# Kernel tuning notes

Measured on AMD Instinct MI355X. Metric: run time of the kernel, lower is better.

## Reference

```python
import jax, jax.numpy as jnp
import numpy as np

N = 60000      # total nodes
D = 300        # feature dim
R = 5          # num relations == num bases
E = 1_000_000  # edges
S = 25000      # last_idx_senses
G = 50000      # last_idx_globals
BATCH = 32


def setup_inputs() -> dict:
    key = jax.random.key(0)
    ks = jax.random.split(key, 12)
    x = jax.random.normal(ks[0], (N, D), dtype=jnp.float32)
    edge_index = jax.random.randint(ks[1], (2, E), 0, N, dtype=jnp.int32)
    edge_type = jax.random.randint(ks[2], (E,), 0, R, dtype=jnp.int32)
    current_node_index = jax.random.randint(ks[3], (BATCH,), 0, N, dtype=jnp.int32)
    scale = 1.0 / np.sqrt(D)
    # RGCNConv basis decomposition params (num_bases == num_relations)
    basis = jax.random.normal(ks[4], (R, D, D), dtype=jnp.float32) * scale
    comp = jax.random.normal(ks[5], (R, R), dtype=jnp.float32) * scale
    root = jax.random.normal(ks[6], (D, D), dtype=jnp.float32) * scale
    bias = jnp.zeros((D,), dtype=jnp.float32)
    # heads
    w_global = jax.random.normal(ks[7], (G - S, D), dtype=jnp.float32) * scale
    b_global = jnp.zeros((G - S,), dtype=jnp.float32)
    w_sense = jax.random.normal(ks[8], (S, D), dtype=jnp.float32) * scale
    b_sense = jnp.zeros((S,), dtype=jnp.float32)
    return {
        "x": x, "edge_index": edge_index, "edge_type": edge_type,
        "current_node_index": current_node_index,
        "basis": basis, "comp": comp, "root": root, "bias": bias,
        "w_global": w_global, "b_global": b_global,
        "w_sense": w_sense, "b_sense": b_sense,
    }


def reference(x, edge_index, edge_type, current_node_index,
              basis, comp, root, bias,
              w_global, b_global, w_sense, b_sense):
    src, dst = edge_index[0], edge_index[1]
    # Combined segment id over (dst node, relation): mean-aggregate source
    # features per (node, relation), then apply the per-relation transform
    # (mean(x_j) @ W_r == mean(x_j @ W_r); matches PyG RGCNConv aggr='mean').
    seg = dst * R + edge_type                      # [E]
    msg_sum = jax.ops.segment_sum(x[src], seg, num_segments=N * R)  # [N*R, D]
    cnt = jax.ops.segment_sum(jnp.ones((E,), jnp.float32), seg, num_segments=N * R)
    mean = msg_sum.reshape(N, R, D) / jnp.maximum(cnt.reshape(N, R, 1), 1.0)
    # basis decomposition: W_r = sum_b comp[r,b] * basis[b]
    W = jnp.einsum('rb,bij->rij', comp, basis)     # [R, D, D]
    agg = jnp.einsum('nrd,rde->ne', mean, W)       # [N, D]
    h = jax.nn.relu(agg + x @ root + bias)         # [N, D]
    hc = h[current_node_index]                     # [B, D]
    logits_global = hc @ w_global.T + b_global     # [B, G-S]
    logits_sense = hc @ w_sense.T + b_sense        # [B, S]
    return (jax.nn.log_softmax(logits_global, axis=-1),
            jax.nn.log_softmax(logits_sense, axis=-1))
```

## Files before the change

### kernel.cpp

```cpp
#include <hip/hip_runtime.h>
#include <hip/hip_bf16.h>
#include <math.h>

#define NN 60000
#define D 300
#define R 5
#define NE 1000000
#define B 32
#define NG 25000
#define NS 25000
#define NROWS 50000
#define HCP 304
#define NBLK 1563

typedef __bf16 bf16x8 __attribute__((ext_vector_type(8)));
typedef float f32x16 __attribute__((ext_vector_type(16)));


__global__ void zero_ws(float4* __restrict__ p) {
    int i = blockIdx.x * 256 + threadIdx.x;
    if (i < 14441) p[i] = float4{0.f, 0.f, 0.f, 0.f};
}

__global__ __launch_bounds__(256) void scan_accum(
        const int* __restrict__ ei, const int* __restrict__ et,
        const int* __restrict__ cur, const float* __restrict__ x,
        float* __restrict__ wsum, float* __restrict__ wcnt) {
    __shared__ unsigned int tbl[32];
    __shared__ int curl[B];
    __shared__ int lcnt;
    __shared__ int2 loc[64];
    int tid = threadIdx.x;
    if (tid < 32) tbl[tid] = 0u;
    if (tid == 0) lcnt = 0;
    __syncthreads();
    if (tid < B) {
        int c = cur[tid];
        curl[tid] = c;
        atomicOr(&tbl[(c >> 5) & 31], 1u << (c & 31));
    }
    __syncthreads();
    long base = ((long)blockIdx.x * 256 + tid) * 4;
    if (base < NE) {
        int ds[4];
        if (base + 4 <= NE) {
            int4 d4 = *(const int4*)(ei + NE + base);
            ds[0] = d4.x; ds[1] = d4.y; ds[2] = d4.z; ds[3] = d4.w;
        } else {
            for (int k = 0; k < 4; ++k) ds[k] = (base + k < NE) ? ei[NE + base + k] : -1;
        }
        #pragma unroll
        for (int k = 0; k < 4; ++k) {
            int dst = ds[k];
            if (dst < 0) continue;
            if (!(tbl[(dst >> 5) & 31] & (1u << (dst & 31)))) continue;
            int e = (int)base + k;
            int r = -1, s = 0;
            for (int b = 0; b < B; ++b) {
                if (dst == curl[b]) {
                    if (r < 0) { r = et[e]; s = ei[e]; }
                    int slot = b * R + r;
                    atomicAdd(&wcnt[slot], 1.0f);
                    int p = atomicAdd(&lcnt, 1);
                    if (p < 64) loc[p] = int2{s, slot};
                }
            }
        }
    }
    __syncthreads();
    int n = lcnt; if (n > 64) n = 64;
    for (int m = 0; m < n; ++m) {
        int2 pr = loc[m];
        const float* xs = x + (long)pr.x * D;
        float* sm = wsum + (long)pr.y * D;
        for (int t = tid; t < D; t += 256) atomicAdd(&sm[t], xs[t]);
    }
}

__global__ __launch_bounds__(320) void rgcn_hc(
        const float* __restrict__ x, const int* __restrict__ cur,
        const float* __restrict__ comp, const float* __restrict__ root,
        const float* __restrict__ basis, const float* __restrict__ bias,
        const float* __restrict__ wsum, const float* __restrict__ wcnt,
        float* __restrict__ hcf, int* __restrict__ done, __bf16* __restrict__ hcb) {
    int kc = blockIdx.x, t = threadIdx.x;
    __shared__ float uL[B * 50];
    __shared__ float cmp[R * R];
    __shared__ float inv[B * R];
    __shared__ int curlS[B];
    __shared__ int lastFlag;
    if (t < R * R) cmp[t] = comp[t];
    if (t < B * R) inv[t] = 1.0f / fmaxf(wcnt[t], 1.0f);
    if (t < B) curlS[t] = cur[t];
    __syncthreads();
    int d0 = kc * 50;
    if (kc < 6) {
        for (int i = t; i < B * 50; i += 320) {
            int b = i / 50, dd = i - b * 50;
            uL[i] = x[(long)curlS[b] * D + d0 + dd];
        }
    } else {
        int g0 = d0 - 300;
        int bb = g0 / 300, t0 = g0 - bb * 300;
        for (int i = t; i < B * 50; i += 320) {
            int b = i / 50, dd = i - b * 50;
            float a = 0.f;
            #pragma unroll
            for (int r = 0; r < R; ++r)
                a = fmaf(cmp[r * R + bb] * inv[b * R + r], wsum[((long)b * R + r) * D + t0 + dd], a);
            uL[i] = a;
        }
    }
    __syncthreads();
    const float* Mb = (kc < 6) ? (root + (long)d0 * D) : (basis + (long)(d0 - 300) * D);
    if (t < D) {
        float acc[B] = {};
        #pragma unroll 5
        for (int i = 0; i < 50; ++i) {
            float m = Mb[(long)i * D + t];
            #pragma unroll
            for (int b = 0; b < B; ++b) acc[b] = fmaf(uL[b * 50 + i], m, acc[b]);
        }
        for (int b = 0; b < B; ++b) atomicAdd(&hcf[b * D + t], acc[b]);
    }
    __syncthreads();
    if (t == 0) {
        __threadfence();
        int p = atomicAdd(done, 1);
        lastFlag = (p == 35);
    }
    __syncthreads();
    if (!lastFlag) return;
    __threadfence();
    for (int i = t; i < B * HCP; i += 320) {
        int b = i / HCP, tt = i - b * HCP;
        float a = 0.f;
        if (tt < D) {
            a = atomicAdd(&hcf[b * D + tt], 0.0f) + bias[tt];
            a = fmaxf(a, 0.f);
        }
        hcb[i] = (__bf16)a;
    }
}

__device__ inline void online_upd(float& m, float& s, float v) {
    if (v > m) { s = s * __expf(m - v) + 1.0f; m = v; }
    else       { s += __expf(v - m); }
}
__device__ inline void online_merge(float& m, float& s, float om, float os) {
    float M = fmaxf(m, om);
    s = s * __expf(m - M) + os * __expf(om - M);
    m = M;
}

__global__ __launch_bounds__(64) void head_gemm_mfma(
    const __bf16* __restrict__ hcb, const float* __restrict__ wg, const float* __restrict__ bg,
    const float* __restrict__ wsn, const float* __restrict__ bsn,
    float* __restrict__ out, float2* __restrict__ pm2) {
    int l = threadIdx.x;
    int j0 = blockIdx.x * 32;
    int lm = l & 31, lh = l >> 5;

    bf16x8 bfrag[19];
    const __bf16* hrow = hcb + lm * HCP + lh * 8;
    #pragma unroll
    for (int s = 0; s < 19; ++s) bfrag[s] = *(const bf16x8*)(hrow + 16 * s);

    int row = j0 + lm; if (row >= NROWS) row = NROWS - 1;
    const float* wrow = ((row < NG) ? (wg + (long)row * D) : (wsn + (long)(row - NG) * D)) + lh * 8;

    f32x16 acc = {};
    #pragma unroll
    for (int s = 0; s < 18; ++s) {
        float4 w0 = *(const float4*)(wrow + 16 * s);
        float4 w1 = *(const float4*)(wrow + 16 * s + 4);
        bf16x8 a;
        a[0] = (__bf16)w0.x; a[1] = (__bf16)w0.y; a[2] = (__bf16)w0.z; a[3] = (__bf16)w0.w;
        a[4] = (__bf16)w1.x; a[5] = (__bf16)w1.y; a[6] = (__bf16)w1.z; a[7] = (__bf16)w1.w;
        acc = __builtin_amdgcn_mfma_f32_32x32x16_bf16(a, bfrag[s], acc, 0, 0, 0);
    }
    {
        float4 w0, w1;
        if (lh == 0) {
            w0 = *(const float4*)(wrow + 288);
            w1 = *(const float4*)(wrow + 292);
        } else {
            w0 = *(const float4*)(wrow + 288);
            w1 = float4{0.f, 0.f, 0.f, 0.f};
        }
        bf16x8 a;
        a[0] = (__bf16)w0.x; a[1] = (__bf16)w0.y; a[2] = (__bf16)w0.z; a[3] = (__bf16)w0.w;
        a[4] = (__bf16)w1.x; a[5] = (__bf16)w1.y; a[6] = (__bf16)w1.z; a[7] = (__bf16)w1.w;
        acc = __builtin_amdgcn_mfma_f32_32x32x16_bf16(a, bfrag[18], acc, 0, 0, 0);
    }

    int b = lm;
    float m0 = -3.0e38f, s0 = 0.f, m1 = -3.0e38f, s1 = 0.f;
    #pragma unroll
    for (int r = 0; r < 16; ++r) {
        int j = j0 + (r & 3) + 8 * (r >> 2) + 4 * lh;
        if (j >= NROWS) continue;
        float bv = (j < NG) ? bg[j] : bsn[j - NG];
        float v = acc[r] + bv;
        float* op = (j < NG) ? (out + (long)b * NG + j)
                             : (out + (long)B * NG + (long)b * NS + (j - NG));
        *op = v;
        if (j < NG) online_upd(m0, s0, v); else online_upd(m1, s1, v);
    }
    float om0 = __shfl_xor(m0, 32), os0 = __shfl_xor(s0, 32);
    float om1 = __shfl_xor(m1, 32), os1 = __shfl_xor(s1, 32);
    online_merge(m0, s0, om0, os0);
    online_merge(m1, s1, om1, os1);
    if (lh == 0) {
        pm2[(long)b * NBLK + blockIdx.x]       = float2{m0, s0};
        pm2[(long)(B + b) * NBLK + blockIdx.x] = float2{m1, s1};
    }
}

__global__ __launch_bounds__(256) void sub_lse(float* __restrict__ out,
                                               const float2* __restrict__ pm2) {
    int row = blockIdx.x / 25, c = blockIdx.x % 25;
    int tid = threadIdx.x;
    const float2* pr = pm2 + (long)row * NBLK;
    float m = -3.0e38f, s = 0.f;
    for (int i = tid; i < NBLK; i += 256) {
        float2 e = pr[i];
        online_merge(m, s, e.x, e.y);
    }
    #pragma unroll
    for (int o = 32; o; o >>= 1) {
        float om = __shfl_xor(m, o), os = __shfl_xor(s, o);
        online_merge(m, s, om, os);
    }
    __shared__ float sm[4], ss[4];
    __shared__ float lseS;
    if ((tid & 63) == 0) { sm[tid >> 6] = m; ss[tid >> 6] = s; }
    __syncthreads();
    if (tid == 0) {
        float M = sm[0], S = ss[0];
        for (int w = 1; w < 4; ++w) online_merge(M, S, sm[w], ss[w]);
        lseS = M + __logf(S);
    }
    __syncthreads();
    float lse = lseS;
    float4* o4 = (float4*)out + (long)row * 6250 + c * 250;
    if (tid < 250) {
        float4 v = o4[tid];
        v.x -= lse; v.y -= lse; v.z -= lse; v.w -= lse;
        o4[tid] = v;
    }
}

extern "C" void kernel_launch(void* const* d_in, const int* in_sizes, int n_in,
                              void* d_out, int out_size, void* d_ws, size_t ws_size,
                              hipStream_t stream) {
    const float* x     = (const float*)d_in[0];
    const int*   ei    = (const int*)d_in[1];
    const int*   et    = (const int*)d_in[2];
    const int*   cur   = (const int*)d_in[3];
    const float* basis = (const float*)d_in[4];
    const float* comp  = (const float*)d_in[5];
    const float* root  = (const float*)d_in[6];
    const float* bias  = (const float*)d_in[7];
    const float* wg    = (const float*)d_in[8];
    const float* bgl   = (const float*)d_in[9];
    const float* wsn   = (const float*)d_in[10];
    const float* bsn   = (const float*)d_in[11];
    float* out  = (float*)d_out;
    float* wsf  = (float*)d_ws;
    float* wsum  = wsf;
    float* wcnt  = wsf + 48000;
    float* hcf   = wsf + 48160;
    int*   done  = (int*)(wsf + 57760);
    __bf16* hcb  = (__bf16*)(wsf + 57764);
    float2* pm2  = (float2*)(wsf + 62628);

    zero_ws<<<57, 256, 0, stream>>>((float4*)d_ws);
    scan_accum<<<977, 256, 0, stream>>>(ei, et, cur, x, wsum, wcnt);
    rgcn_hc<<<36, 320, 0, stream>>>(x, cur, comp, root, basis, bias, wsum, wcnt, hcf, done, hcb);
    head_gemm_mfma<<<NBLK, 64, 0, stream>>>(hcb, wg, bgl, wsn, bsn, out, pm2);
    sub_lse<<<1600, 256, 0, stream>>>(out, pm2);
}
```

Baseline: 81.70 us.

## Restructure RGCN/head pipeline: finer rgcn split, fused bias-ReLU into head, separate LSE reduction

The rgcn_hc stage now uses 72 blocks over 25-row chunks instead of 36 over 50, which doubles parallelism. The last-block epilogue with its done counter and threadfences is removed. Bias+ReLU and the bf16 conversion of hc move into the head GEMM, which stages them in shared memory and runs 4 waves per block. The per-row LSE reduction is split out into its own 64-block kernel so sub_lse no longer recomputes it 25 times per row. This adds one more launch and redundant hc conversion in each of the 391 head blocks.

```diff
diff --git a/kernel.cpp b/kernel.cpp
--- a/kernel.cpp
+++ b/kernel.cpp
@@ -2,7 +2,6 @@
 #include <hip/hip_bf16.h>
 #include <math.h>
 
-#define NN 60000
 #define D 300
 #define R 5
 #define NE 1000000
@@ -10,16 +9,25 @@
 #define NG 25000
 #define NS 25000
 #define NROWS 50000
-#define HCP 304
 #define NBLK 1563
 
 typedef __bf16 bf16x8 __attribute__((ext_vector_type(8)));
 typedef float f32x16 __attribute__((ext_vector_type(16)));
 
 
+__device__ __forceinline__ void online_upd(float& m, float& s, float v) {
+    if (v > m) { s = s * __expf(m - v) + 1.0f; m = v; }
+    else       { s += __expf(v - m); }
+}
+__device__ __forceinline__ void online_merge(float& m, float& s, float om, float os) {
+    float M = fmaxf(m, om);
+    s = s * __expf(m - M) + os * __expf(om - M);
+    m = M;
+}
+
 __global__ void zero_ws(float4* __restrict__ p) {
     int i = blockIdx.x * 256 + threadIdx.x;
-    if (i < 14441) p[i] = float4{0.f, 0.f, 0.f, 0.f};
+    if (i < 14440) p[i] = float4{0.f, 0.f, 0.f, 0.f};
 }
 
 __global__ __launch_bounds__(256) void scan_accum(
@@ -34,35 +42,30 @@
     if (tid < 32) tbl[tid] = 0u;
     if (tid == 0) lcnt = 0;
     __syncthreads();
-    if (tid < B) {
-        int c = cur[tid];
-        curl[tid] = c;
-        atomicOr(&tbl[(c >> 5) & 31], 1u << (c & 31));
-    }
+    if (tid < B) { int c = cur[tid]; curl[tid] = c; atomicOr(&tbl[(c >> 5) & 31], 1u << (c & 31)); }
     __syncthreads();
     long base = ((long)blockIdx.x * 256 + tid) * 4;
     if (base < NE) {
-        int ds[4];
+        int ds4[4];
         if (base + 4 <= NE) {
             int4 d4 = *(const int4*)(ei + NE + base);
-            ds[0] = d4.x; ds[1] = d4.y; ds[2] = d4.z; ds[3] = d4.w;
+            ds4[0] = d4.x; ds4[1] = d4.y; ds4[2] = d4.z; ds4[3] = d4.w;
         } else {
-            for (int k = 0; k < 4; ++k) ds[k] = (base + k < NE) ? ei[NE + base + k] : -1;
+            for (int k = 0; k < 4; ++k) ds4[k] = (base + k < NE) ? ei[NE + base + k] : -1;
         }
         #pragma unroll
         for (int k = 0; k < 4; ++k) {
-            int dst = ds[k];
+            int dst = ds4[k];
             if (dst < 0) continue;
             if (!(tbl[(dst >> 5) & 31] & (1u << (dst & 31)))) continue;
             int e = (int)base + k;
-            int r = -1, s = 0;
+            int r = -1, src = 0;
             for (int b = 0; b < B; ++b) {
                 if (dst == curl[b]) {
-                    if (r < 0) { r = et[e]; s = ei[e]; }
-                    int slot = b * R + r;
-                    atomicAdd(&wcnt[slot], 1.0f);
+                    if (r < 0) { r = et[e]; src = ei[e]; }
+                    atomicAdd(&wcnt[b * R + r], 1.0f);
                     int p = atomicAdd(&lcnt, 1);
-                    if (p < 64) loc[p] = int2{s, slot};
+                    if (p < 64) loc[p] = int2{src, b * R + r};
                 }
             }
         }
@@ -80,92 +83,71 @@
 __global__ __launch_bounds__(320) void rgcn_hc(
         const float* __restrict__ x, const int* __restrict__ cur,
         const float* __restrict__ comp, const float* __restrict__ root,
-        const float* __restrict__ basis, const float* __restrict__ bias,
-        const float* __restrict__ wsum, const float* __restrict__ wcnt,
-        float* __restrict__ hcf, int* __restrict__ done, __bf16* __restrict__ hcb) {
+        const float* __restrict__ basis, const float* __restrict__ wsum,
+        const float* __restrict__ wcnt, float* __restrict__ hcf) {
     int kc = blockIdx.x, t = threadIdx.x;
-    __shared__ float uL[B * 50];
+    __shared__ float uL[800];
+    __shared__ float inv[B * R];
     __shared__ float cmp[R * R];
-    __shared__ float inv[B * R];
-    __shared__ int curlS[B];
-    __shared__ int lastFlag;
-    if (t < R * R) cmp[t] = comp[t];
     if (t < B * R) inv[t] = 1.0f / fmaxf(wcnt[t], 1.0f);
-    if (t < B) curlS[t] = cur[t];
-    __syncthreads();
-    int d0 = kc * 50;
-    if (kc < 6) {
-        for (int i = t; i < B * 50; i += 320) {
-            int b = i / 50, dd = i - b * 50;
-            uL[i] = x[(long)curlS[b] * D + d0 + dd];
+    if (t >= 160 && t < 160 + R * R) cmp[t - 160] = comp[t - 160];
+    __syncthreads();
+    int d0 = kc * 25;
+    if (d0 < 300) {
+        for (int i = t; i < 800; i += 320) {
+            int b = i / 25, dd = i - b * 25;
+            uL[i] = x[(long)cur[b] * D + d0 + dd];
         }
     } else {
         int g0 = d0 - 300;
         int bb = g0 / 300, t0 = g0 - bb * 300;
-        for (int i = t; i < B * 50; i += 320) {
-            int b = i / 50, dd = i - b * 50;
+        for (int i = t; i < 800; i += 320) {
+            int b = i / 25, dd = i - b * 25;
             float a = 0.f;
             #pragma unroll
             for (int r = 0; r < R; ++r)
-                a = fmaf(cmp[r * R + bb] * inv[b * R + r], wsum[((long)b * R + r) * D + t0 + dd], a);
+                a = fmaf(cmp[r * R + bb] * inv[b * R + r], wsum[(long)(b * R + r) * D + t0 + dd], a);
             uL[i] = a;
         }
     }
     __syncthreads();
-    const float* Mb = (kc < 6) ? (root + (long)d0 * D) : (basis + (long)(d0 - 300) * D);
     if (t < D) {
+        const float* Mb = (d0 < 300) ? (root + (long)d0 * D) : (basis + (long)(d0 - 300) * D);
         float acc[B] = {};
         #pragma unroll 5
-        for (int i = 0; i < 50; ++i) {
+        for (int i = 0; i < 25; ++i) {
             float m = Mb[(long)i * D + t];
             #pragma unroll
-            for (int b = 0; b < B; ++b) acc[b] = fmaf(uL[b * 50 + i], m, acc[b]);
+            for (int b = 0; b < B; ++b) acc[b] = fmaf(uL[b * 25 + i], m, acc[b]);
         }
         for (int b = 0; b < B; ++b) atomicAdd(&hcf[b * D + t], acc[b]);
     }
-    __syncthreads();
-    if (t == 0) {
-        __threadfence();
-        int p = atomicAdd(done, 1);
-        lastFlag = (p == 35);
-    }
-    __syncthreads();
-    if (!lastFlag) return;
-    __threadfence();
-    for (int i = t; i < B * HCP; i += 320) {
-        int b = i / HCP, tt = i - b * HCP;
-        float a = 0.f;
-        if (tt < D) {
-            a = atomicAdd(&hcf[b * D + tt], 0.0f) + bias[tt];
-            a = fmaxf(a, 0.f);
-        }
-        hcb[i] = (__bf16)a;
-    }
-}
-
-__device__ inline void online_upd(float& m, float& s, float v) {
-    if (v > m) { s = s * __expf(m - v) + 1.0f; m = v; }
-    else       { s += __expf(v - m); }
-}
-__device__ inline void online_merge(float& m, float& s, float om, float os) {
-    float M = fmaxf(m, om);
-    s = s * __expf(m - M) + os * __expf(om - M);
-    m = M;
-}
-
-__global__ __launch_bounds__(64) void head_gemm_mfma(
-    const __bf16* __restrict__ hcb, const float* __restrict__ wg, const float* __restrict__ bg,
+}
+
+__global__ __launch_bounds__(256) void head_gemm_mfma(
+    const float* __restrict__ hcf, const float* __restrict__ bias,
+    const float* __restrict__ wg, const float* __restrict__ bg,
     const float* __restrict__ wsn, const float* __restrict__ bsn,
     float* __restrict__ out, float2* __restrict__ pm2) {
-    int l = threadIdx.x;
-    int j0 = blockIdx.x * 32;
-    int lm = l & 31, lh = l >> 5;
+    __shared__ __bf16 hcbL[32 * 304];
+    int tid = threadIdx.x;
+    for (int i = tid; i < 32 * 304; i += 256) {
+        int b = i / 304, kk = i - b * 304;
+        float v = 0.f;
+        if (kk < D) v = fmaxf(hcf[b * D + kk] + bias[kk], 0.f);
+        hcbL[i] = (__bf16)v;
+    }
+    __syncthreads();
+    int wid = tid >> 6, l = tid & 63, lm = l & 31, lh = l >> 5;
+    int tile = blockIdx.x * 4 + wid;
+    if (tile >= NBLK) return;
 
     bf16x8 bfrag[19];
-    const __bf16* hrow = hcb + lm * HCP + lh * 8;
+    const __bf16* hrow = hcbL + lm * 304 + lh * 8;
     #pragma unroll
     for (int s = 0; s < 19; ++s) bfrag[s] = *(const bf16x8*)(hrow + 16 * s);
 
+    int j0 = tile * 32;
     int row = j0 + lm; if (row >= NROWS) row = NROWS - 1;
     const float* wrow = ((row < NG) ? (wg + (long)row * D) : (wsn + (long)(row - NG) * D)) + lh * 8;
 
@@ -175,22 +157,16 @@
         float4 w0 = *(const float4*)(wrow + 16 * s);
         float4 w1 = *(const float4*)(wrow + 16 * s + 4);
         bf16x8 a;
-        a[0] = (__bf16)w0.x; a[1] = (__bf16)w0.y; a[2] = (__bf16)w0.z; a[3] = (__bf16)w0.w;
-        a[4] = (__bf16)w1.x; a[5] = (__bf16)w1.y; a[6] = (__bf16)w1.z; a[7] = (__bf16)w1.w;
+        a[0]=(__bf16)w0.x; a[1]=(__bf16)w0.y; a[2]=(__bf16)w0.z; a[3]=(__bf16)w0.w;
+        a[4]=(__bf16)w1.x; a[5]=(__bf16)w1.y; a[6]=(__bf16)w1.z; a[7]=(__bf16)w1.w;
         acc = __builtin_amdgcn_mfma_f32_32x32x16_bf16(a, bfrag[s], acc, 0, 0, 0);
     }
     {
-        float4 w0, w1;
-        if (lh == 0) {
-            w0 = *(const float4*)(wrow + 288);
-            w1 = *(const float4*)(wrow + 292);
-        } else {
-            w0 = *(const float4*)(wrow + 288);
-            w1 = float4{0.f, 0.f, 0.f, 0.f};
-        }
+        float4 w0 = *(const float4*)(wrow + 288);
+        float4 w1 = (lh == 0) ? *(const float4*)(wrow + 292) : float4{0.f, 0.f, 0.f, 0.f};
         bf16x8 a;
-        a[0] = (__bf16)w0.x; a[1] = (__bf16)w0.y; a[2] = (__bf16)w0.z; a[3] = (__bf16)w0.w;
-        a[4] = (__bf16)w1.x; a[5] = (__bf16)w1.y; a[6] = (__bf16)w1.z; a[7] = (__bf16)w1.w;
+        a[0]=(__bf16)w0.x; a[1]=(__bf16)w0.y; a[2]=(__bf16)w0.z; a[3]=(__bf16)w0.w;
+        a[4]=(__bf16)w1.x; a[5]=(__bf16)w1.y; a[6]=(__bf16)w1.z; a[7]=(__bf16)w1.w;
         acc = __builtin_amdgcn_mfma_f32_32x32x16_bf16(a, bfrag[18], acc, 0, 0, 0);
     }
 
@@ -212,43 +188,39 @@
     online_merge(m0, s0, om0, os0);
     online_merge(m1, s1, om1, os1);
     if (lh == 0) {
-        pm2[(long)b * NBLK + blockIdx.x]       = float2{m0, s0};
-        pm2[(long)(B + b) * NBLK + blockIdx.x] = float2{m1, s1};
-    }
-}
-
-__global__ __launch_bounds__(256) void sub_lse(float* __restrict__ out,
-                                               const float2* __restrict__ pm2) {
-    int row = blockIdx.x / 25, c = blockIdx.x % 25;
-    int tid = threadIdx.x;
-    const float2* pr = pm2 + (long)row * NBLK;
+        pm2[(long)b * NBLK + tile]       = float2{m0, s0};
+        pm2[(long)(B + b) * NBLK + tile] = float2{m1, s1};
+    }
+}
+
+__global__ __launch_bounds__(256) void lse_red(const float2* __restrict__ pm2,
+                                               float* __restrict__ lse) {
+    int rw = blockIdx.x, tid = threadIdx.x;
+    const float2* pr = pm2 + (long)rw * NBLK;
     float m = -3.0e38f, s = 0.f;
-    for (int i = tid; i < NBLK; i += 256) {
-        float2 e = pr[i];
-        online_merge(m, s, e.x, e.y);
-    }
+    for (int i = tid; i < NBLK; i += 256) { float2 e = pr[i]; online_merge(m, s, e.x, e.y); }
     #pragma unroll
     for (int o = 32; o; o >>= 1) {
         float om = __shfl_xor(m, o), os = __shfl_xor(s, o);
         online_merge(m, s, om, os);
     }
     __shared__ float sm[4], ss[4];
-    __shared__ float lseS;
     if ((tid & 63) == 0) { sm[tid >> 6] = m; ss[tid >> 6] = s; }
     __syncthreads();
     if (tid == 0) {
         float M = sm[0], S = ss[0];
         for (int w = 1; w < 4; ++w) online_merge(M, S, sm[w], ss[w]);
-        lseS = M + __logf(S);
-    }
-    __syncthreads();
-    float lse = lseS;
-    float4* o4 = (float4*)out + (long)row * 6250 + c * 250;
-    if (tid < 250) {
-        float4 v = o4[tid];
-        v.x -= lse; v.y -= lse; v.z -= lse; v.w -= lse;
-        o4[tid] = v;
-    }
+        lse[rw] = M + __logf(S);
+    }
+}
+
+__global__ __launch_bounds__(256) void sub_lse(float* __restrict__ out,
+                                               const float* __restrict__ lse) {
+    int rw = blockIdx.x / 25, c = blockIdx.x % 25;
+    float l = lse[rw];
+    float4* o4 = (float4*)out + (long)rw * 6250 + c * 250;
+    int tid = threadIdx.x;
+    if (tid < 250) { float4 v = o4[tid]; v.x -= l; v.y -= l; v.z -= l; v.w -= l; o4[tid] = v; }
 }
 
 extern "C" void kernel_launch(void* const* d_in, const int* in_sizes, int n_in,
@@ -268,16 +240,16 @@
     const float* bsn   = (const float*)d_in[11];
     float* out  = (float*)d_out;
     float* wsf  = (float*)d_ws;
-    float* wsum  = wsf;
-    float* wcnt  = wsf + 48000;
-    float* hcf   = wsf + 48160;
-    int*   done  = (int*)(wsf + 57760);
-    __bf16* hcb  = (__bf16*)(wsf + 57764);
-    float2* pm2  = (float2*)(wsf + 62628);
+    float*  wsum = wsf;
+    float*  wcnt = wsf + 48000;
+    float*  hcf  = wsf + 48160;
+    float2* pm2  = (float2*)(wsf + 57760);
+    float*  lse  = wsf + 257824;
 
     zero_ws<<<57, 256, 0, stream>>>((float4*)d_ws);
     scan_accum<<<977, 256, 0, stream>>>(ei, et, cur, x, wsum, wcnt);
-    rgcn_hc<<<36, 320, 0, stream>>>(x, cur, comp, root, basis, bias, wsum, wcnt, hcf, done, hcb);
-    head_gemm_mfma<<<NBLK, 64, 0, stream>>>(hcb, wg, bgl, wsn, bsn, out, pm2);
-    sub_lse<<<1600, 256, 0, stream>>>(out, pm2);
-}
+    rgcn_hc<<<72, 320, 0, stream>>>(x, cur, comp, root, basis, wsum, wcnt, hcf);
+    head_gemm_mfma<<<391, 256, 0, stream>>>(hcf, bias, wg, bgl, wsn, bsn, out, pm2);
+    lse_red<<<64, 256, 0, stream>>>(pm2, lse);
+    sub_lse<<<1600, 256, 0, stream>>>(out, lse);
+}
```

Result: faster. 73.94 us (-9.5%).
